# Optimization experiments

Measured on AMD Instinct MI355X. Metric: run time of the kernel, lower is better.

## Reference

```python
import jax, jax.numpy as jnp
import numpy as np

EMB, QK, V, H = 1024, 64, 64, 16
B, S = 4, 2048


def setup_inputs() -> dict:
    key = jax.random.key(0)
    ks = jax.random.split(key, 8)
    sc = 0.02
    x_q = jax.random.normal(ks[0], (B, S, EMB), jnp.float32)
    x_k_v = jax.random.normal(ks[1], (B, S, EMB), jnp.float32)
    # causal mask: True means masked (matches torch masked_fill)
    causal = ~jnp.tril(jnp.ones((S, S), dtype=bool))
    attn_mask = jnp.broadcast_to(causal, (B, S, S))
    w_q = jax.random.normal(ks[2], (H * QK, EMB), jnp.float32) * sc
    b_q = jnp.zeros((H * QK,), jnp.float32)
    w_k = jax.random.normal(ks[3], (H * QK, EMB), jnp.float32) * sc
    b_k = jnp.zeros((H * QK,), jnp.float32)
    w_v = jax.random.normal(ks[4], (H * V, EMB), jnp.float32) * sc
    b_v = jnp.zeros((H * V,), jnp.float32)
    return {"x_q": x_q, "x_k_v": x_k_v, "attn_mask": attn_mask,
            "w_q": w_q, "b_q": b_q, "w_k": w_k, "b_k": b_k, "w_v": w_v, "b_v": b_v}


def reference(x_q, x_k_v, attn_mask, w_q, b_q, w_k, b_k, w_v, b_v):
    Bq, Sq, _ = x_q.shape
    Skv = x_k_v.shape[1]
    q = (x_q @ w_q.T + b_q).reshape(Bq, Sq, H, QK).transpose(0, 2, 1, 3)   # [B,H,Sq,QK]
    k = (x_k_v @ w_k.T + b_k).reshape(Bq, Skv, H, QK).transpose(0, 2, 1, 3)  # [B,H,Skv,QK]
    v = (x_k_v @ w_v.T + b_v).reshape(Bq, Skv, H, V).transpose(0, 2, 1, 3)   # [B,H,Skv,V]
    attn = jnp.einsum('bhqd,bhkd->bhqk', q, k) / jnp.sqrt(jnp.float32(QK))
    attn = jnp.where(attn_mask[:, None, :, :], jnp.float32(-1e9), attn)
    attn = jax.nn.softmax(attn, axis=-1)
    z = jnp.einsum('bhqk,bhkv->bhqv', attn, v)        # [B,H,Sq,V]
    z = z.transpose(0, 2, 1, 3).reshape(Bq, Sq, H * V)
    return z
```

## Files before the change

### kernel.cpp

```cpp
#include <hip/hip_runtime.h>

#define B_    4
#define H_    16
#define S_    2048
#define EMB_  1024
#define D_    64

typedef __attribute__((ext_vector_type(4))) float f32x4;
typedef __attribute__((ext_vector_type(8))) short frag_ab;
typedef unsigned short ushort_t;

__device__ __forceinline__ unsigned short f2bf(float f) {
    unsigned int u = __float_as_uint(f);
    unsigned int r = u + 0x7fffu + ((u >> 16) & 1u);
    return (unsigned short)(r >> 16);
}
__device__ __forceinline__ unsigned short f2bf_fast(float f) {
    return (unsigned short)((__float_as_uint(f) + 0x8000u) >> 16);
}

__device__ __forceinline__ void gld16(const void* g, void* l) {
    __builtin_amdgcn_global_load_lds(
        (const __attribute__((address_space(1))) void*)g,
        (__attribute__((address_space(3))) void*)l, 16, 0, 0);
}

#define SCOL(lane) ((((lane) & 7) ^ (((lane) >> 3) & 7)) * 8)

__global__ void cvt_all(const float* __restrict__ s0, const float* __restrict__ s1,
                        const float* __restrict__ s2, const float* __restrict__ s3,
                        const float* __restrict__ s4,
                        ushort_t* __restrict__ d0, ushort_t* __restrict__ d1,
                        ushort_t* __restrict__ d2, ushort_t* __restrict__ d3,
                        ushort_t* __restrict__ d4) {
    const int b = blockIdx.x;
    const float* src; ushort_t* dst; int i;
    if (b < 3072) {
        const int z = b >> 10;
        src = (z == 0) ? s0 : (z == 1 ? s1 : s2);
        dst = (z == 0) ? d0 : (z == 1 ? d1 : d2);
        i = (b & 1023) * 256 + threadIdx.x;
    } else {
        const int b2 = b - 3072;
        const int z = b2 >> 13;
        src = z ? s4 : s3;
        dst = z ? d4 : d3;
        i = (b2 & 8191) * 256 + threadIdx.x;
    }
    float4 f = ((const float4*)src)[i];
    ushort4 o;
    o.x = f2bf(f.x); o.y = f2bf(f.y); o.z = f2bf(f.z); o.w = f2bf(f.w);
    ((ushort4*)dst)[i] = o;
}

__global__ __launch_bounds__(256) void qkv_gemm(
    const ushort_t* __restrict__ xq,
    const ushort_t* __restrict__ xkv,
    const ushort_t* __restrict__ wq,
    const ushort_t* __restrict__ wk,
    const ushort_t* __restrict__ wv,
    const float* __restrict__ bq,
    const float* __restrict__ bk,
    const float* __restrict__ bv,
    ushort_t* __restrict__ qo,
    ushort_t* __restrict__ ko,
    ushort_t* __restrict__ vto)
{
    __shared__ ushort_t As[2][128 * 64];
    __shared__ ushort_t Bs[2][128 * 64];

    const int id = blockIdx.x;
    const int xcd = id & 7, j = id >> 3;
    const int big_t   = xcd * 8 + (j & 7);
    const int small_t = (j >> 3) & 7;
    const int z       = j >> 6;

    const float* bias = (z == 0) ? bq : (z == 1 ? bk : bv);
    const float scale = (z == 0) ? 0.125f * 1.44269504089f : 1.0f;

    const int tid = threadIdx.x;
    const int w = tid >> 6, lane = tid & 63, quad = lane >> 4, l16 = lane & 15;
    const int wm = w & 1, wn = w >> 1;
    const int scol = SCOL(lane);

    int m0, n0;
    const ushort_t *Aptr, *Bptr;
    if (z == 2) {
        m0 = big_t * 128;  n0 = small_t * 128;
        Aptr = xkv;        Bptr = wv;
    } else {
        m0 = small_t * 128; n0 = big_t * 128;
        Aptr = (z == 0) ? wq : wk;
        Bptr = (z == 0) ? xq : xkv;
    }

    f32x4 acc[4][4];
#pragma unroll
    for (int i = 0; i < 4; ++i)
#pragma unroll
        for (int j2 = 0; j2 < 4; ++j2) acc[i][j2] = (f32x4){0.f, 0.f, 0.f, 0.f};

    const ushort_t* pa = Aptr + (size_t)(m0 + w * 32 + (lane >> 3)) * EMB_ + scol;
    const ushort_t* pb = Bptr + (size_t)(n0 + w * 32 + (lane >> 3)) * EMB_ + scol;

    auto stage = [&](int bsel, int kt) {
        const int k0 = kt * 64;
#pragma unroll
        for (int i = 0; i < 4; ++i) {
            const int base = w * 32 + i * 8;
            gld16(pa + (size_t)(i * 8) * EMB_ + k0, &As[bsel][base * 64]);
            gld16(pb + (size_t)(i * 8) * EMB_ + k0, &Bs[bsel][base * 64]);
        }
    };

    const int key = l16 & 7;
    stage(0, 0);
    for (int kt = 0; kt < 16; ++kt) {
        __syncthreads();
        if (kt < 15) stage((kt + 1) & 1, kt + 1);
        const int bsel = kt & 1;

#pragma unroll
        for (int c = 0; c < 2; ++c) {
            const int boff = ((c * 4 + quad) ^ key) * 8;
            frag_ab a[4], bfr[4];
#pragma unroll
            for (int t = 0; t < 4; ++t) {
                a[t]   = *(const frag_ab*)&As[bsel][(wm * 64 + t * 16 + l16) * 64 + boff];
                bfr[t] = *(const frag_ab*)&Bs[bsel][(wn * 64 + t * 16 + l16) * 64 + boff];
            }
#pragma unroll
            for (int tm = 0; tm < 4; ++tm)
#pragma unroll
                for (int tn = 0; tn < 4; ++tn)
                    acc[tm][tn] = __builtin_amdgcn_mfma_f32_16x16x32_bf16(
                        a[tm], bfr[tn], acc[tm][tn], 0, 0, 0);
        }
    }

    if (z == 2) {
#pragma unroll
        for (int tn = 0; tn < 4; ++tn) {
            int n = n0 + wn * 64 + tn * 16 + l16;
            float bval = bias[n];
            int hh = n >> 6, dd = n & 63;
#pragma unroll
            for (int tm = 0; tm < 4; ++tm) {
                int m = m0 + wm * 64 + tm * 16 + quad * 4;
                int bb = m >> 11, ss = m & (S_ - 1);
                union { ushort4 v; ushort_t u[4]; } pk;
#pragma unroll
                for (int r = 0; r < 4; ++r) pk.u[r] = f2bf(acc[tm][tn][r] + bval);
                *(ushort4*)&vto[(((size_t)bb * H_ + hh) * D_ + dd) * S_ + ss] = pk.v;
            }
        }
    } else {
        ushort_t* ob = (z == 0) ? qo : ko;
#pragma unroll
        for (int tm = 0; tm < 4; ++tm) {
            int mb = m0 + wm * 64 + tm * 16 + quad * 4;
            int hh = mb >> 6, dd = mb & 63;
            float4 bv4 = *(const float4*)&bias[mb];
#pragma unroll
            for (int tn = 0; tn < 4; ++tn) {
                int n = n0 + wn * 64 + tn * 16 + l16;
                int bb = n >> 11, ss = n & (S_ - 1);
                union { ushort4 v; ushort_t u[4]; } pk;
                pk.u[0] = f2bf((acc[tm][tn][0] + bv4.x) * scale);
                pk.u[1] = f2bf((acc[tm][tn][1] + bv4.y) * scale);
                pk.u[2] = f2bf((acc[tm][tn][2] + bv4.z) * scale);
                pk.u[3] = f2bf((acc[tm][tn][3] + bv4.w) * scale);
                *(ushort4*)&ob[(((size_t)bb * H_ + hh) * S_ + ss) * D_ + dd] = pk.v;
            }
        }
    }
}

__global__ __launch_bounds__(256) void attn_kernel(
    const ushort_t* __restrict__ qg,
    const ushort_t* __restrict__ kg,
    const ushort_t* __restrict__ vtg,
    float* __restrict__ out)
{
    __shared__ ushort_t Kt[2][64 * 64];
    __shared__ ushort_t Vt[2][64 * 64];
    __shared__ ushort_t Pb[4][32 * 64];

    const int tid = threadIdx.x;
    const int w = tid >> 6, lane = tid & 63, quad = lane >> 4, l16 = lane & 15;
    const int scol = SCOL(lane);

    const int id = blockIdx.x;
    const int rr = id >> 3;
    const int bh = (id & 7) + 8 * (rr & 7);
    const int qi = 15 - (rr >> 3);
    const int q0 = qi * 128;
    const int b = bh >> 4, h = bh & 15;

    const ushort_t* qp  = qg  + (size_t)bh * S_ * D_;
    const ushort_t* kp  = kg  + (size_t)bh * S_ * D_;
    const ushort_t* vtp = vtg + (size_t)bh * D_ * S_;

    frag_ab aq[2][2];
#pragma unroll
    for (int rg = 0; rg < 2; ++rg) {
        const ushort_t* qr = qp + (size_t)(q0 + rg * 64 + w * 16 + l16) * D_;
        aq[rg][0] = *(const frag_ab*)(qr + quad * 8);
        aq[rg][1] = *(const frag_ab*)(qr + 32 + quad * 8);
    }

    float psum[2][4];
    f32x4 o[2][4];
#pragma unroll
    for (int rg = 0; rg < 2; ++rg)
#pragma unroll
        for (int r = 0; r < 4; ++r) psum[rg][r] = 0.f;
#pragma unroll
    for (int rg = 0; rg < 2; ++rg)
#pragma unroll
        for (int t = 0; t < 4; ++t) o[rg][t] = (f32x4){0.f, 0.f, 0.f, 0.f};

    ushort_t* Pw = &Pb[w][0];
    const int last = 2 * qi + 1;

    auto stage = [&](int bsel, int kt) {
#pragma unroll
        for (int i = 0; i < 2; ++i) {
            const int base = w * 16 + i * 8;
            gld16(kp  + (size_t)(kt * 64 + base + (lane >> 3)) * D_ + scol,
                  &Kt[bsel][base * 64]);
            gld16(vtp + (size_t)(base + (lane >> 3)) * S_ + kt * 64 + scol,
                  &Vt[bsel][base * 64]);
        }
    };

    const int key = l16 & 7;
    stage(0, 0);
    for (int kt = 0; kt <= last; ++kt) {
        __syncthreads();
        if (kt < last) stage((kt + 1) & 1, kt + 1);
        const int bsel = kt & 1;

        frag_ab bk[4][2], bv[4][2];
#pragma unroll
        for (int t = 0; t < 4; ++t) {
#pragma unroll
            for (int hf = 0; hf < 2; ++hf) {
                const int off = (t * 16 + l16) * 64 + ((hf * 4 + quad) ^ key) * 8;
                bk[t][hf] = *(const frag_ab*)&Kt[bsel][off];
                bv[t][hf] = *(const frag_ab*)&Vt[bsel][off];
            }
        }

#pragma unroll
        for (int rg = 0; rg < 2; ++rg) {
            if (rg == 0 && kt == last) continue;
            const bool diag = (kt == 2 * qi + rg);
            f32x4 scf[4];
            __builtin_amdgcn_s_setprio(1);
#pragma unroll
            for (int tn = 0; tn < 4; ++tn) {
                f32x4 sc = (f32x4){0.f, 0.f, 0.f, 0.f};
                sc = __builtin_amdgcn_mfma_f32_16x16x32_bf16(aq[rg][0], bk[tn][0], sc, 0, 0, 0);
                sc = __builtin_amdgcn_mfma_f32_16x16x32_bf16(aq[rg][1], bk[tn][1], sc, 0, 0, 0);
                scf[tn] = sc;
            }
            __builtin_amdgcn_s_setprio(0);
            if (diag) {
#pragma unroll
                for (int tn = 0; tn < 4; ++tn) {
                    int kcol = kt * 64 + tn * 16 + l16;
#pragma unroll
                    for (int r = 0; r < 4; ++r) {
                        int qrow = q0 + rg * 64 + w * 16 + quad * 4 + r;
                        if (kcol > qrow) scf[tn][r] = -1e30f;
                    }
                }
            }
#pragma unroll
            for (int r = 0; r < 4; ++r) {
                const int prow = rg * 16 + quad * 4 + r;
                const int rowoff = prow * 64 + (l16 & 7);
                const int pkey = prow & 7;
#pragma unroll
                for (int tn = 0; tn < 4; ++tn) {
                    float p = __builtin_amdgcn_exp2f(scf[tn][r]);
                    psum[rg][r] += p;
                    Pw[rowoff + ((tn * 2 + (l16 >> 3)) ^ pkey) * 8] = f2bf_fast(p);
                }
            }
        }
        asm volatile("s_waitcnt lgkmcnt(0)" ::: "memory");
#pragma unroll
        for (int rg = 0; rg < 2; ++rg) {
            if (rg == 0 && kt == last) continue;
            const int poff = (rg * 16 + l16) * 64;
            frag_ab ap0 = *(const frag_ab*)&Pw[poff + ((0 + quad) ^ key) * 8];
            frag_ab ap1 = *(const frag_ab*)&Pw[poff + ((4 + quad) ^ key) * 8];
            __builtin_amdgcn_s_setprio(1);
#pragma unroll
            for (int tv = 0; tv < 4; ++tv) {
                o[rg][tv] = __builtin_amdgcn_mfma_f32_16x16x32_bf16(ap0, bv[tv][0], o[rg][tv], 0, 0, 0);
                o[rg][tv] = __builtin_amdgcn_mfma_f32_16x16x32_bf16(ap1, bv[tv][1], o[rg][tv], 0, 0, 0);
            }
            __builtin_amdgcn_s_setprio(0);
        }
    }

    float* ob = out + (size_t)b * S_ * (H_ * D_) + h * D_;
#pragma unroll
    for (int rg = 0; rg < 2; ++rg) {
#pragma unroll
        for (int r = 0; r < 4; ++r) {
            float s = psum[rg][r];
            s += __shfl_xor(s, 1);
            s += __shfl_xor(s, 2);
            s += __shfl_xor(s, 4);
            s += __shfl_xor(s, 8);
            float inv = 1.0f / s;
            int srow = q0 + rg * 64 + w * 16 + quad * 4 + r;
#pragma unroll
            for (int tv = 0; tv < 4; ++tv)
                ob[(size_t)srow * (H_ * D_) + tv * 16 + l16] = o[rg][tv][r] * inv;
        }
    }
}

extern "C" void kernel_launch(void* const* d_in, const int* in_sizes, int n_in,
                              void* d_out, int out_size, void* d_ws, size_t ws_size,
                              hipStream_t stream) {
    const float* x_q  = (const float*)d_in[0];
    const float* x_kv = (const float*)d_in[1];
    const float* w_q  = (const float*)d_in[3];
    const float* b_q  = (const float*)d_in[4];
    const float* w_k  = (const float*)d_in[5];
    const float* b_k  = (const float*)d_in[6];
    const float* w_v  = (const float*)d_in[7];
    const float* b_v  = (const float*)d_in[8];
    float* out = (float*)d_out;

    ushort_t* ws  = (ushort_t*)d_ws;
    ushort_t* wqb = ws;
    ushort_t* wkb = wqb + 1048576;
    ushort_t* wvb = wkb + 1048576;
    ushort_t* xqb  = wvb + 1048576;
    ushort_t* xkvb = xqb + 8388608;
    ushort_t* qb   = xkvb + 8388608;
    ushort_t* kb   = qb + 8388608;
    ushort_t* vtb  = kb + 8388608;

    cvt_all<<<19456, 256, 0, stream>>>(
        w_q, w_k, w_v, x_q, x_kv, wqb, wkb, wvb, xqb, xkvb);
    qkv_gemm<<<1536, 256, 0, stream>>>(
        xqb, xkvb, wqb, wkb, wvb, b_q, b_k, b_v, qb, kb, vtb);
    attn_kernel<<<1024, 256, 0, stream>>>(qb, kb, vtb, out);
}
```

Baseline: 291.1 us.

## Replace double-buffered LDS staging with single-buffer load-sync-compute loops

Both the QKV GEMM and attention kernels drop the two-stage LDS ping-pong buffers in favour of a single buffer that is loaded, synchronised, and then consumed each iteration. This halves LDS use per block, which may allow more resident blocks per CU. In exchange, global-to-LDS loads no longer overlap with MFMA compute, and each iteration adds a second barrier.

```diff
diff --git a/kernel.cpp b/kernel.cpp
--- a/kernel.cpp
+++ b/kernel.cpp
@@ -66,8 +66,8 @@
     ushort_t* __restrict__ ko,
     ushort_t* __restrict__ vto)
 {
-    __shared__ ushort_t As[2][128 * 64];
-    __shared__ ushort_t Bs[2][128 * 64];
+    __shared__ ushort_t As[128 * 64];
+    __shared__ ushort_t Bs[128 * 64];
 
     const int id = blockIdx.x;
     const int xcd = id & 7, j = id >> 3;
@@ -103,22 +103,21 @@
     const ushort_t* pa = Aptr + (size_t)(m0 + w * 32 + (lane >> 3)) * EMB_ + scol;
     const ushort_t* pb = Bptr + (size_t)(n0 + w * 32 + (lane >> 3)) * EMB_ + scol;
 
-    auto stage = [&](int bsel, int kt) {
+    auto stage = [&](int kt) {
         const int k0 = kt * 64;
 #pragma unroll
         for (int i = 0; i < 4; ++i) {
             const int base = w * 32 + i * 8;
-            gld16(pa + (size_t)(i * 8) * EMB_ + k0, &As[bsel][base * 64]);
-            gld16(pb + (size_t)(i * 8) * EMB_ + k0, &Bs[bsel][base * 64]);
+            gld16(pa + (size_t)(i * 8) * EMB_ + k0, &As[base * 64]);
+            gld16(pb + (size_t)(i * 8) * EMB_ + k0, &Bs[base * 64]);
         }
     };
 
     const int key = l16 & 7;
-    stage(0, 0);
     for (int kt = 0; kt < 16; ++kt) {
         __syncthreads();
-        if (kt < 15) stage((kt + 1) & 1, kt + 1);
-        const int bsel = kt & 1;
+        stage(kt);
+        __syncthreads();
 
 #pragma unroll
         for (int c = 0; c < 2; ++c) {
@@ -126,8 +125,8 @@
             frag_ab a[4], bfr[4];
 #pragma unroll
             for (int t = 0; t < 4; ++t) {
-                a[t]   = *(const frag_ab*)&As[bsel][(wm * 64 + t * 16 + l16) * 64 + boff];
-                bfr[t] = *(const frag_ab*)&Bs[bsel][(wn * 64 + t * 16 + l16) * 64 + boff];
+                a[t]   = *(const frag_ab*)&As[(wm * 64 + t * 16 + l16) * 64 + boff];
+                bfr[t] = *(const frag_ab*)&Bs[(wn * 64 + t * 16 + l16) * 64 + boff];
             }
 #pragma unroll
             for (int tm = 0; tm < 4; ++tm)
@@ -182,8 +181,8 @@
     const ushort_t* __restrict__ vtg,
     float* __restrict__ out)
 {
-    __shared__ ushort_t Kt[2][64 * 64];
-    __shared__ ushort_t Vt[2][64 * 64];
+    __shared__ ushort_t Kt[64 * 64];
+    __shared__ ushort_t Vt[64 * 64];
     __shared__ ushort_t Pb[4][32 * 64];
 
     const int tid = threadIdx.x;
@@ -223,23 +222,22 @@
     ushort_t* Pw = &Pb[w][0];
     const int last = 2 * qi + 1;
 
-    auto stage = [&](int bsel, int kt) {
+    auto stage = [&](int kt) {
 #pragma unroll
         for (int i = 0; i < 2; ++i) {
             const int base = w * 16 + i * 8;
             gld16(kp  + (size_t)(kt * 64 + base + (lane >> 3)) * D_ + scol,
-                  &Kt[bsel][base * 64]);
+                  &Kt[base * 64]);
             gld16(vtp + (size_t)(base + (lane >> 3)) * S_ + kt * 64 + scol,
-                  &Vt[bsel][base * 64]);
+                  &Vt[base * 64]);
         }
     };
 
     const int key = l16 & 7;
-    stage(0, 0);
     for (int kt = 0; kt <= last; ++kt) {
         __syncthreads();
-        if (kt < last) stage((kt + 1) & 1, kt + 1);
-        const int bsel = kt & 1;
+        stage(kt);
+        __syncthreads();
 
         frag_ab bk[4][2], bv[4][2];
 #pragma unroll
@@ -247,8 +245,8 @@
 #pragma unroll
             for (int hf = 0; hf < 2; ++hf) {
                 const int off = (t * 16 + l16) * 64 + ((hf * 4 + quad) ^ key) * 8;
-                bk[t][hf] = *(const frag_ab*)&Kt[bsel][off];
-                bv[t][hf] = *(const frag_ab*)&Vt[bsel][off];
+                bk[t][hf] = *(const frag_ab*)&Kt[off];
+                bv[t][hf] = *(const frag_ab*)&Vt[off];
             }
         }
 
```

Measured after the change: 296.3 us. About the same (+1.8%).
